# Optimization experiments

Hardware: AMD Instinct MI355X
Metric: run time of the kernel (lower is better)

Reference implementation:

```python
import jax, jax.numpy as jnp
import numpy as np

N_USERS = 100000
N_ITEMS = 50000
D = 128          # n_factors
L = 200          # hist_len
B = 2048
SIGMA = 0.1      # hyper_approx (posterior lognormal scale)
PRIOR = 1.0      # hyper_prior (prior lognormal scale)
TAU = 4.0
EPS = 1e-8
LN_EPS = 1e-5


def _layernorm(x, gamma, beta):
    m = jnp.mean(x, axis=-1, keepdims=True)
    v = jnp.var(x, axis=-1, keepdims=True)
    return (x - m) * jax.lax.rsqrt(v + LN_EPS) * gamma + beta


def setup_inputs() -> dict:
    key = jax.random.key(0)
    ks = jax.random.split(key, 20)
    user_idx = jax.random.randint(ks[0], (B,), 0, N_USERS, dtype=jnp.int32)
    item_idx = jax.random.randint(ks[1], (B,), 0, N_ITEMS, dtype=jnp.int32)
    # user_hist buffer: per-user ragged history padded with N_ITEMS
    lengths = jax.random.randint(ks[2], (N_USERS,), 1, L + 1, dtype=jnp.int32)
    raw_hist = jax.random.randint(ks[3], (N_USERS, L), 0, N_ITEMS, dtype=jnp.int32)
    pos = jnp.arange(L, dtype=jnp.int32)
    user_hist = jnp.where(pos[None, :] < lengths[:, None], raw_hist, N_ITEMS).astype(jnp.int32)
    # embeddings (padding rows zeroed, std=0.01 init)
    user_embed = 0.01 * jax.random.normal(ks[4], (N_USERS + 1, D), dtype=jnp.float32)
    user_embed = user_embed.at[N_USERS].set(0.0)
    item_embed = 0.01 * jax.random.normal(ks[5], (N_ITEMS + 1, D), dtype=jnp.float32)
    item_embed = item_embed.at[N_ITEMS].set(0.0)
    s = 1.0 / np.sqrt(D)
    W_i = s * jax.random.normal(ks[6], (D, D), dtype=jnp.float32)
    W_h = s * jax.random.normal(ks[7], (D, D), dtype=jnp.float32)
    # BAM 'concat' (additive) score params: v^T tanh(Wq q + Wk k)
    Wq = s * jax.random.normal(ks[8], (D, D), dtype=jnp.float32)
    Wk = s * jax.random.normal(ks[9], (D, D), dtype=jnp.float32)
    v_attn = s * jax.random.normal(ks[10], (D,), dtype=jnp.float32)
    pred_W = s * jax.random.normal(ks[11], (D,), dtype=jnp.float32)
    pred_b = jnp.zeros((), dtype=jnp.float32)
    gamma_u = jnp.ones((D,), jnp.float32); beta_u = jnp.zeros((D,), jnp.float32)
    gamma_i = jnp.ones((D,), jnp.float32); beta_i = jnp.zeros((D,), jnp.float32)
    # reparameterization noise (forward uses stochastic=True)
    noise_u = jax.random.normal(ks[12], (B, L), dtype=jnp.float32)
    noise_i = jax.random.normal(ks[13], (B, L), dtype=jnp.float32)
    return dict(user_idx=user_idx, item_idx=item_idx, user_hist=user_hist,
                user_embed=user_embed, item_embed=item_embed, W_i=W_i, W_h=W_h,
                Wq=Wq, Wk=Wk, v_attn=v_attn, pred_W=pred_W, pred_b=pred_b,
                gamma_u=gamma_u, beta_u=beta_u, gamma_i=gamma_i, beta_i=beta_i,
                noise_u=noise_u, noise_i=noise_i)


def reference(user_idx, item_idx, user_hist, user_embed, item_embed, W_i, W_h,
              Wq, Wk, v_attn, pred_W, pred_b, gamma_u, beta_u, gamma_i, beta_i,
              noise_u, noise_i):
    maskf_dummy = None  # (placeholder, no-op)
    hist = user_hist[user_idx]                                   # (B, L) int
    mask = (hist != item_idx[:, None]) & (hist != N_ITEMS)       # (B, L) bool
    maskf = mask.astype(jnp.float32)

    u_id = user_embed[user_idx]                                  # (B, D)
    t_raw = item_embed[item_idx]                                 # (B, D)
    h_raw = item_embed[hist]                                     # (B, L, D)
    t_id = t_raw @ W_i.T                                         # W_i(target)
    h_id = h_raw @ W_h.T                                         # W_h(hist)

    def bam(q, K, V, noise):
        # additive ('concat') scoring: v . tanh(q Wq + K Wk), temperature tau
        h = jnp.tanh((q @ Wq.T)[:, None, :] + jnp.einsum('bld,ed->ble', K, Wk))
        scores = jnp.einsum('ble,e->bl', h, v_attn) / TAU        # (B, L)
        scores = jnp.where(mask, scores, -1e9)
        phi = jax.nn.softmax(scores, axis=-1)                    # (B, L)
        mu = jnp.log(phi + EPS)
        w = jnp.exp(mu + SIGMA * noise) * maskf                  # lognormal sample
        attn = w / (jnp.sum(w, axis=-1, keepdims=True) + EPS)
        out = jnp.einsum('bl,bld->bd', attn, V)                  # (B, D)
        # KL( LN(mu, SIGMA) || LN(0, PRIOR) ) over valid positions
        kl_el = jnp.log(PRIOR / SIGMA) + (SIGMA ** 2 + mu ** 2) / (2.0 * PRIOR ** 2) - 0.5
        kl = jnp.sum(kl_el * maskf) / (jnp.sum(maskf) + EPS)
        return out, kl

    u_hist, kl_u = bam(u_id, h_id, h_id, noise_u)
    i_hist, kl_i = bam(t_id, h_id, h_id, noise_i)
    u = _layernorm(u_hist * u_id, gamma_u, beta_u)
    i = _layernorm(i_hist * t_id, gamma_i, beta_i)
    logit = (u * i) @ pred_W + pred_b                            # (B,)
    return logit, 0.5 * (kl_u + kl_i)
```

## Files before the change

kernel.cpp:

```cpp
#include <hip/hip_runtime.h>

#define B_ 2048
#define L_ 200
#define D_ 128
#define NITEMS 50000

typedef __attribute__((ext_vector_type(8))) short short8v;
typedef __attribute__((ext_vector_type(4))) float floatx4;
typedef __attribute__((ext_vector_type(4))) int intx4;

__device__ __forceinline__ short f2bf(float f) {
    union { float f; unsigned u; } v;
    v.f = f;
    unsigned r = v.u + 0x7FFFu + ((v.u >> 16) & 1u);
    return (short)(r >> 16);
}

__device__ __forceinline__ float tanh5(float x) {
    const float x2 = x * x;
    const float p = __builtin_fmaf(x2, 0.13333333f, -0.33333333f);
    return __builtin_fmaf(x * x2, p, x);
}

__device__ __forceinline__ float wave_sum(float v) {
#pragma unroll
    for (int m = 32; m >= 1; m >>= 1) v += __shfl_xor(v, m, 64);
    return v;
}

__device__ __forceinline__ void gload_lds16(const short* g, short* l) {
    __builtin_amdgcn_global_load_lds(
        (const __attribute__((address_space(1))) void*)g,
        (__attribute__((address_space(3))) void*)l, 16, 0, 0);
}

__device__ __forceinline__ intx4 ds_read16(const short* p) {
    intx4 d;
    asm volatile("ds_read_b128 %0, %1"
                 : "=v"(d)
                 : "v"((const __attribute__((address_space(3))) short*)p));
    return d;
}

__global__ __launch_bounds__(256) void k01(const float* __restrict__ Wk,
                                           const float* __restrict__ Wh,
                                           short* __restrict__ Mbf,
                                           const float* __restrict__ src,
                                           short* __restrict__ dst, int n8) {
    const int t = threadIdx.x;
    if (blockIdx.x < 128) {
        __shared__ float wk[128];
        const int e = blockIdx.x;
        if (t < 128) wk[t] = Wk[e * 128 + t];
        __syncthreads();
        if (t < 128) {
            float s = 0.f;
#pragma unroll 4
            for (int d = 0; d < 128; ++d) s += wk[d] * Wh[d * 128 + t];
            Mbf[e * 128 + t] = f2bf(s);
        }
        return;
    }
    const int i = (blockIdx.x - 128) * 256 + t;
    if (i >= n8) return;
    const float4 f0 = *reinterpret_cast<const float4*>(src + i * 8);
    const float4 f1 = *reinterpret_cast<const float4*>(src + i * 8 + 4);
    short8v w;
    w[0] = f2bf(f0.x); w[1] = f2bf(f0.y); w[2] = f2bf(f0.z); w[3] = f2bf(f0.w);
    w[4] = f2bf(f1.x); w[5] = f2bf(f1.y); w[6] = f2bf(f1.z); w[7] = f2bf(f1.w);
    *reinterpret_cast<short8v*>(dst + i * 8) = w;
}

__global__ __launch_bounds__(256) void k2_prep(
    const int* __restrict__ user_idx, const int* __restrict__ item_idx,
    const int* __restrict__ user_hist, const float* __restrict__ user_embed,
    const float* __restrict__ item_embed, const float* __restrict__ W_i,
    const float* __restrict__ Wq, float* __restrict__ uid_o,
    float* __restrict__ tid_o, float* __restrict__ qu_o, float* __restrict__ qt_o,
    int* __restrict__ hist_o) {
    const int bb = blockIdx.x * 4, t = threadIdx.x;
    __shared__ float uid_s[4][128], traw_s[4][128], tid_s[4][128];
    __shared__ int uis[4], iis[4];
    if (t < 4) {
        uis[t] = user_idx[bb + t];
        iis[t] = item_idx[bb + t];
    }
    __syncthreads();
#pragma unroll
    for (int c = 0; c < 2; ++c) {
        const int idx = c * 256 + t;
        const int bs = idx >> 7, e = idx & 127;
        const float uv = user_embed[(long)uis[bs] * 128 + e];
        uid_s[bs][e] = uv;
        traw_s[bs][e] = item_embed[(long)iis[bs] * 128 + e];
        uid_o[(bb + bs) * 128 + e] = uv;
    }
    for (int l0 = t; l0 < 800; l0 += 256) {
        const int bs = (l0 >= 200) + (l0 >= 400) + (l0 >= 600);
        hist_o[bb * 200 + l0] = user_hist[(long)uis[bs] * 200 + (l0 - bs * 200)];
    }
    __syncthreads();
    {
        const int half = t >> 7, e = t & 127;
        const float* Wrow = (half ? Wq : W_i) + e * 128;
        float acc[4] = {0.f, 0.f, 0.f, 0.f};
        for (int c = 0; c < 128; c += 4) {
            const float4 w = *reinterpret_cast<const float4*>(Wrow + c);
#pragma unroll
            for (int k = 0; k < 4; ++k) {
                const float4 s = half ? *reinterpret_cast<const float4*>(&uid_s[k][c])
                                      : *reinterpret_cast<const float4*>(&traw_s[k][c]);
                acc[k] += w.x * s.x + w.y * s.y + w.z * s.z + w.w * s.w;
            }
        }
#pragma unroll
        for (int k = 0; k < 4; ++k) {
            if (half) qu_o[(bb + k) * 128 + e] = acc[k];
            else {
                tid_s[k][e] = acc[k];
                tid_o[(bb + k) * 128 + e] = acc[k];
            }
        }
    }
    __syncthreads();
    {
        const int half = t >> 7, e = t & 127;
        const float* Wrow = Wq + e * 128;
        float acc[2] = {0.f, 0.f};
        for (int c = 0; c < 128; c += 4) {
            const float4 w = *reinterpret_cast<const float4*>(Wrow + c);
#pragma unroll
            for (int k = 0; k < 2; ++k) {
                const float4 s = *reinterpret_cast<const float4*>(&tid_s[half * 2 + k][c]);
                acc[k] += w.x * s.x + w.y * s.y + w.z * s.z + w.w * s.w;
            }
        }
#pragma unroll
        for (int k = 0; k < 2; ++k) qt_o[(bb + half * 2 + k) * 128 + e] = acc[k];
    }
}

__global__ __launch_bounds__(512) void k345(
    const short* __restrict__ Mbf, const short* __restrict__ item_bf,
    const int* __restrict__ hist_g, const int* __restrict__ item_idx,
    const float* __restrict__ qu_, const float* __restrict__ qt_,
    const float* __restrict__ v_attn, const float* __restrict__ noise_u,
    const float* __restrict__ noise_i, const float* __restrict__ W_h,
    const float* __restrict__ uid, const float* __restrict__ tid,
    const float* __restrict__ gamma_u, const float* __restrict__ beta_u,
    const float* __restrict__ gamma_i, const float* __restrict__ beta_i,
    const float* __restrict__ pred_W, const float* __restrict__ pred_b,
    float* __restrict__ klu, float* __restrict__ kli, float* __restrict__ msm,
    float* __restrict__ out) {
    __shared__ __align__(16) short M_lds[8][4][4][16][8];
    __shared__ __align__(16) char scratch[32768];
    __shared__ float q_lds[2][2][128];
    __shared__ float v_lds[128];
    __shared__ int hgs[400];
    __shared__ float scL[2 * 400];
    __shared__ float attL[2 * 400];
    __shared__ float red[8];

    const int t = threadIdx.x, blk = blockIdx.x;
    const int b0 = blk * 2;
    const int ii0 = item_idx[b0], ii1 = item_idx[b0 + 1];

#pragma unroll
    for (int c4 = 0; c4 < 4; ++c4) {
        const int flat = c4 * 512 + t;
        const int lo = flat & 15, g = (flat >> 4) & 3, ks = (flat >> 6) & 3, t8 = flat >> 8;
        *reinterpret_cast<short8v*>(&M_lds[t8][ks][g][lo][0]) =
            *reinterpret_cast<const short8v*>(Mbf + (t8 * 16 + lo) * 128 + ks * 32 + g * 8);
    }
    {
        const int bs = t >> 8, side = (t >> 7) & 1, e = t & 127;
        q_lds[bs][side][e] =
            side ? qt_[(b0 + bs) * 128 + e] : qu_[(b0 + bs) * 128 + e];
    }
    if (t < 128) v_lds[t] = v_attn[t];
    if (t < 400) hgs[t] = hist_g[blk * 400 + t];
    __syncthreads();

    const int wid = t >> 6, lane = t & 63;
    const int lo = lane & 15, hi = lane >> 4;

    {
        const int nt = (wid == 7) ? 4 : 3;
        short* wbase = reinterpret_cast<short*>(scratch) + wid * 2048;
        const char* itemc = (const char*)item_bf;

        int ro[4];
#pragma unroll
        for (int i = 0; i < 4; ++i) {
            const int lt = wid * 3 + ((i < 3) ? i : 3);
            ro[i] = hgs[min(lt, 24) * 16 + lo];
        }
        auto stage = [&](int i) {
            const char* rp = itemc + ((long)ro[i] << 8) + hi * 16;
#pragma unroll
            for (int ks = 0; ks < 4; ++ks)
                gload_lds16((const short*)(rp + ks * 64), wbase + ks * 512);
        };

        stage(0);
        for (int i = 0; i < nt; ++i) {
            asm volatile("s_waitcnt vmcnt(0)" ::: "memory");
            __builtin_amdgcn_sched_barrier(0);
            const short* pb = wbase + hi * 128 + lo * 8;
            intx4 r0 = ds_read16(pb);
            intx4 r1 = ds_read16(pb + 512);
            intx4 r2 = ds_read16(pb + 1024);
            intx4 r3 = ds_read16(pb + 1536);
            asm volatile("s_waitcnt lgkmcnt(0)" ::: "memory");
            __builtin_amdgcn_sched_barrier(0);
            short8v f[4];
            f[0] = __builtin_bit_cast(short8v, r0);
            f[1] = __builtin_bit_cast(short8v, r1);
            f[2] = __builtin_bit_cast(short8v, r2);
            f[3] = __builtin_bit_cast(short8v, r3);
            if (i + 1 < nt) stage(i + 1);
            __builtin_amdgcn_sched_barrier(0);

            const int lr = (wid * 3 + i) * 16 + lo;
            const int bs = lr >= 200;
            float su = 0.f, si = 0.f;
#pragma unroll
            for (int h2 = 0; h2 < 2; ++h2) {
                floatx4 acc[4];
#pragma unroll
                for (int q4 = 0; q4 < 4; ++q4) acc[q4] = (floatx4){0.f, 0.f, 0.f, 0.f};
#pragma unroll
                for (int ks = 0; ks < 4; ++ks)
#pragma unroll
                    for (int q4 = 0; q4 < 4; ++q4)
                        acc[q4] = __builtin_amdgcn_mfma_f32_16x16x32_bf16(
                            *reinterpret_cast<const short8v*>(&M_lds[h2 * 4 + q4][ks][hi][lo][0]),
                            f[ks], acc[q4], 0, 0, 0);
#pragma unroll
                for (int q4 = 0; q4 < 4; ++q4) {
                    const int t8 = h2 * 4 + q4;
                    const floatx4 vv = *reinterpret_cast<const floatx4*>(&v_lds[t8 * 16 + hi * 4]);
                    const floatx4 qa = *reinterpret_cast<const floatx4*>(&q_lds[bs][0][t8 * 16 + hi * 4]);
                    const floatx4 qb = *reinterpret_cast<const floatx4*>(&q_lds[bs][1][t8 * 16 + hi * 4]);
#pragma unroll
                    for (int rg = 0; rg < 4; ++rg) {
                        su = __builtin_fmaf(vv[rg], tanh5(qa[rg] + acc[q4][rg]), su);
                        si = __builtin_fmaf(vv[rg], tanh5(qb[rg] + acc[q4][rg]), si);
                    }
                }
            }
            su += __shfl_xor(su, 16, 64);
            su += __shfl_xor(su, 32, 64);
            si += __shfl_xor(si, 16, 64);
            si += __shfl_xor(si, 32, 64);
            if (hi == 0) {
                scL[lr] = su * 0.25f;
                scL[400 + lr] = si * 0.25f;
            }
        }
    }
    __syncthreads();

    if (wid < 4) {
        const int bs = wid & 1, side = wid >> 1;
        const int bb = b0 + bs;
        const int iiv = bs ? ii1 : ii0;
        const float* nz = (side ? noise_i : noise_u) + bb * L_;
        const float* scl = scL + side * 400 + bs * 200;
        const int* hrow = hgs + bs * 200;

        float mk[4], s2[4];
        float msl = 0.f, esum = 0.f;
#pragma unroll
        for (int k = 0; k < 4; ++k) {
            const int l = lane + 64 * k;
            const int hv = (l < L_) ? hrow[l] : NITEMS;
            mk[k] = (l < L_ && hv != iiv && hv != NITEMS) ? 1.f : 0.f;
            msl += mk[k];
            const float s = (mk[k] > 0.5f) ? scl[(l < L_) ? l : 0] : -1e9f;
            s2[k] = s * 1.4426950f;
            esum += exp2f(s2[k]);
        }
        const float msum = wave_sum(msl);
        float Z = wave_sum(esum);
        Z = fmaxf(Z, 1e-37f);
        const float z2 = log2f(Z);

        float wv[4], wsum = 0.f, klsum = 0.f;
#pragma unroll
        for (int k = 0; k < 4; ++k) {
            const int l = lane + 64 * k;
            const int lm = (l < L_) ? l : 0;
            const float d = s2[k] - z2;
            wv[k] = exp2f(__builtin_fmaf(nz[lm], 0.14426950f, d)) * mk[k];
            wsum += wv[k];
            klsum += (1.8075851f + 0.2402265f * d * d) * mk[k];
        }
        const float Zw = wave_sum(wsum);
        const float kls = wave_sum(klsum);
        const float invZw = 1.f / (Zw + 1e-8f);
#pragma unroll
        for (int k = 0; k < 4; ++k) {
            const int l = lane + 64 * k;
            if (l < L_) attL[side * 400 + bs * 200 + l] = wv[k] * invZw;
        }
        if (lane == 0) {
            if (side == 0) { klu[bb] = kls; msm[bb] = msum; }
            else kli[bb] = kls;
        }
    }
    __syncthreads();

    float* P = reinterpret_cast<float*>(scratch);
    {
        const int bs = wid >> 2, rg = wid & 3, c2 = lane;
        const float* a0p = attL + bs * 200;
        const float* a1p = attL + 400 + bs * 200;
        const int* hrow = hgs + bs * 200;
        float s00 = 0.f, s01 = 0.f, s10 = 0.f, s11 = 0.f;
#pragma unroll
        for (int c = 0; c < 2; ++c) {
            const int lb = rg * 50 + c * 25;
            unsigned hv[25];
#pragma unroll
            for (int j = 0; j < 25; ++j)
                hv[j] = *reinterpret_cast<const unsigned*>(
                    item_bf + (long)hrow[lb + j] * 128 + c2 * 2);
#pragma unroll
            for (int j = 0; j < 25; ++j) {
                const float h0 = __uint_as_float(hv[j] << 16);
                const float h1 = __uint_as_float(hv[j] & 0xffff0000u);
                const float a0 = a0p[lb + j], a1 = a1p[lb + j];
                s00 += a0 * h0; s01 += a0 * h1;
                s10 += a1 * h0; s11 += a1 * h1;
            }
        }
        P[((bs * 2 + 0) * 4 + rg) * 128 + c2 * 2] = s00;
        P[((bs * 2 + 0) * 4 + rg) * 128 + c2 * 2 + 1] = s01;
        P[((bs * 2 + 1) * 4 + rg) * 128 + c2 * 2] = s10;
        P[((bs * 2 + 1) * 4 + rg) * 128 + c2 * 2 + 1] = s11;
    }
    __syncthreads();

    const int bs3 = t >> 8, side3 = (t >> 7) & 1, tl = t & 127;
    const int grp = t >> 7;
    {
        const int gidx = (bs3 * 2 + side3) * 4;
        float a = P[(gidx + 0) * 128 + tl] + P[(gidx + 1) * 128 + tl] +
                  P[(gidx + 2) * 128 + tl] + P[(gidx + 3) * 128 + tl];
        __syncthreads();
        P[2048 + grp * 128 + tl] = a;
    }
    __syncthreads();

    float x;
    {
        const float* vsrc = P + 2048 + grp * 128;
        float o = 0.f;
#pragma unroll 2
        for (int c = 0; c < 128; c += 4) {
            const float4 w = *reinterpret_cast<const float4*>(&W_h[tl * 128 + c]);
            o += w.x * vsrc[c] + w.y * vsrc[c + 1] + w.z * vsrc[c + 2] + w.w * vsrc[c + 3];
        }
        x = o * (side3 ? tid[(b0 + bs3) * 128 + tl] : uid[(b0 + bs3) * 128 + tl]);
    }
    const float v1 = wave_sum(x);
    if (lane == 0) red[wid] = v1;
    __syncthreads();
    const float mean = (red[grp * 2] + red[grp * 2 + 1]) * (1.f / 128.f);
    const float d = x - mean;
    const float v2 = wave_sum(d * d);
    __syncthreads();
    if (lane == 0) red[wid] = v2;
    __syncthreads();
    const float var = (red[grp * 2] + red[grp * 2 + 1]) * (1.f / 128.f);
    const float gmm = side3 ? gamma_i[tl] : gamma_u[tl];
    const float bta = side3 ? beta_i[tl] : beta_u[tl];
    const float uin = d * rsqrtf(var + 1e-5f) * gmm + bta;
    __syncthreads();
    P[2560 + grp * 128 + tl] = uin;
    __syncthreads();
    float p = 0.f;
    if (t < 256) {
        const int bs = t >> 7, tl2 = t & 127;
        p = P[2560 + (bs * 2 + 0) * 128 + tl2] * P[2560 + (bs * 2 + 1) * 128 + tl2] *
            pred_W[tl2];
    }
    const float v3 = wave_sum(p);
    if (lane == 0 && wid < 4) red[4 + wid] = v3;
    __syncthreads();
    if (t == 0) out[b0] = red[4] + red[5] + pred_b[0];
    if (t == 1) out[b0 + 1] = red[6] + red[7] + pred_b[0];
}

__global__ __launch_bounds__(256) void k6_kl(const float* __restrict__ klu,
                                             const float* __restrict__ kli,
                                             const float* __restrict__ msm,
                                             float* __restrict__ out) {
    __shared__ float red[4];
    const int t = threadIdx.x;
    float su = 0.f, si = 0.f, sm = 0.f;
    for (int b = t; b < B_; b += 256) {
        su += klu[b];
        si += kli[b];
        sm += msm[b];
    }
    su = wave_sum(su);
    si = wave_sum(si);
    sm = wave_sum(sm);
    __syncthreads();
    if ((t & 63) == 0) red[t >> 6] = su;
    __syncthreads();
    su = red[0] + red[1] + red[2] + red[3];
    __syncthreads();
    if ((t & 63) == 0) red[t >> 6] = si;
    __syncthreads();
    si = red[0] + red[1] + red[2] + red[3];
    __syncthreads();
    if ((t & 63) == 0) red[t >> 6] = sm;
    __syncthreads();
    sm = red[0] + red[1] + red[2] + red[3];
    if (t == 0) {
        const float inv = 1.f / (sm + 1e-8f);
        out[0] = 0.5f * (su * inv + si * inv);
    }
}

extern "C" void kernel_launch(void* const* d_in, const int* in_sizes, int n_in,
                              void* d_out, int out_size, void* d_ws, size_t ws_size,
                              hipStream_t stream) {
    const int* user_idx = (const int*)d_in[0];
    const int* item_idx = (const int*)d_in[1];
    const int* user_hist = (const int*)d_in[2];
    const float* user_embed = (const float*)d_in[3];
    const float* item_embed = (const float*)d_in[4];
    const float* W_i = (const float*)d_in[5];
    const float* W_h = (const float*)d_in[6];
    const float* Wq = (const float*)d_in[7];
    const float* Wk = (const float*)d_in[8];
    const float* v_attn = (const float*)d_in[9];
    const float* pred_W = (const float*)d_in[10];
    const float* pred_b = (const float*)d_in[11];
    const float* gamma_u = (const float*)d_in[12];
    const float* beta_u = (const float*)d_in[13];
    const float* gamma_i = (const float*)d_in[14];
    const float* beta_i = (const float*)d_in[15];
    const float* noise_u = (const float*)d_in[16];
    const float* noise_i = (const float*)d_in[17];
    float* out = (float*)d_out;

    char* ws = (char*)d_ws;
    size_t off = 0;
    auto alloc = [&](size_t bytes) -> void* {
        void* p = ws + off;
        off = (off + bytes + 255) & ~(size_t)255;
        return p;
    };
    short* Mbf     = (short*)alloc(128 * 128 * 2);
    short* item_bf = (short*)alloc((size_t)(NITEMS + 1) * 128 * 2);
    float* uid = (float*)alloc((size_t)B_ * 128 * 4);
    float* tid = (float*)alloc((size_t)B_ * 128 * 4);
    float* qu  = (float*)alloc((size_t)B_ * 128 * 4);
    float* qt  = (float*)alloc((size_t)B_ * 128 * 4);
    int* hg    = (int*)alloc((size_t)B_ * L_ * 4);
    float* klu = (float*)alloc((size_t)B_ * 4);
    float* kli = (float*)alloc((size_t)B_ * 4);
    float* msm = (float*)alloc((size_t)B_ * 4);

    const int n8 = (NITEMS + 1) * 128 / 8;
    const int ncvt = (n8 + 255) / 256;
    k01<<<128 + ncvt, 256, 0, stream>>>(Wk, W_h, Mbf, item_embed, item_bf, n8);
    k2_prep<<<B_ / 4, 256, 0, stream>>>(user_idx, item_idx, user_hist, user_embed,
                                        item_embed, W_i, Wq, uid, tid, qu, qt, hg);
    k345<<<B_ / 2, 512, 0, stream>>>(Mbf, item_bf, hg, item_idx, qu, qt, v_attn,
                                     noise_u, noise_i, W_h, uid, tid, gamma_u, beta_u,
                                     gamma_i, beta_i, pred_W, pred_b, klu, kli, msm, out);
    k6_kl<<<1, 256, 0, stream>>>(klu, kli, msm, out + B_);
}
```

Baseline: 103.6 us.

## Merge prep kernels, prefetch history tiles early, single-pass layernorm stats

Merges the weight/item-conversion kernel and the per-batch prep kernel into one launch, removing a kernel boundary. In the main kernel, the first history-row tile is issued before the Mbf/q LDS setup, and half of the value-gather loads are hoisted ahead of the softmax phase so their latency overlaps other work. Layernorm now computes mean and E[x^2] in one reduction instead of two, dropping several barriers. The one-pass variance is less numerically robust, and the hoisted gather arrays add register pressure.

```diff
diff --git a/kernel.cpp b/kernel.cpp
--- a/kernel.cpp
+++ b/kernel.cpp
@@ -42,12 +42,18 @@
     return d;
 }
 
-__global__ __launch_bounds__(256) void k01(const float* __restrict__ Wk,
-                                           const float* __restrict__ Wh,
-                                           short* __restrict__ Mbf,
-                                           const float* __restrict__ src,
-                                           short* __restrict__ dst, int n8) {
+__global__ __launch_bounds__(256) void kprep(
+    const float* __restrict__ Wk, const float* __restrict__ Wh,
+    short* __restrict__ Mbf, const float* __restrict__ item_embed,
+    short* __restrict__ item_bf, int n8,
+    const int* __restrict__ user_idx, const int* __restrict__ item_idx,
+    const int* __restrict__ user_hist, const float* __restrict__ user_embed,
+    const float* __restrict__ W_i, const float* __restrict__ Wq,
+    float* __restrict__ uid_o, float* __restrict__ tid_o,
+    float* __restrict__ qu_o, float* __restrict__ qt_o, int* __restrict__ hist_o) {
     const int t = threadIdx.x;
+    const int ncvt = (n8 + 255) >> 8;
+
     if (blockIdx.x < 128) {
         __shared__ float wk[128];
         const int e = blockIdx.x;
@@ -61,24 +67,18 @@
         }
         return;
     }
-    const int i = (blockIdx.x - 128) * 256 + t;
-    if (i >= n8) return;
-    const float4 f0 = *reinterpret_cast<const float4*>(src + i * 8);
-    const float4 f1 = *reinterpret_cast<const float4*>(src + i * 8 + 4);
-    short8v w;
-    w[0] = f2bf(f0.x); w[1] = f2bf(f0.y); w[2] = f2bf(f0.z); w[3] = f2bf(f0.w);
-    w[4] = f2bf(f1.x); w[5] = f2bf(f1.y); w[6] = f2bf(f1.z); w[7] = f2bf(f1.w);
-    *reinterpret_cast<short8v*>(dst + i * 8) = w;
-}
-
-__global__ __launch_bounds__(256) void k2_prep(
-    const int* __restrict__ user_idx, const int* __restrict__ item_idx,
-    const int* __restrict__ user_hist, const float* __restrict__ user_embed,
-    const float* __restrict__ item_embed, const float* __restrict__ W_i,
-    const float* __restrict__ Wq, float* __restrict__ uid_o,
-    float* __restrict__ tid_o, float* __restrict__ qu_o, float* __restrict__ qt_o,
-    int* __restrict__ hist_o) {
-    const int bb = blockIdx.x * 4, t = threadIdx.x;
+    if (blockIdx.x < 128 + ncvt) {
+        const int i = (blockIdx.x - 128) * 256 + t;
+        if (i >= n8) return;
+        const float4 f0 = *reinterpret_cast<const float4*>(item_embed + i * 8);
+        const float4 f1 = *reinterpret_cast<const float4*>(item_embed + i * 8 + 4);
+        short8v w;
+        w[0] = f2bf(f0.x); w[1] = f2bf(f0.y); w[2] = f2bf(f0.z); w[3] = f2bf(f0.w);
+        w[4] = f2bf(f1.x); w[5] = f2bf(f1.y); w[6] = f2bf(f1.z); w[7] = f2bf(f1.w);
+        *reinterpret_cast<short8v*>(item_bf + i * 8) = w;
+        return;
+    }
+    const int bb = (blockIdx.x - 128 - ncvt) * 4;
     __shared__ float uid_s[4][128], traw_s[4][128], tid_s[4][128];
     __shared__ int uis[4], iis[4];
     if (t < 4) {
@@ -159,18 +159,36 @@
     __shared__ int hgs[400];
     __shared__ float scL[2 * 400];
     __shared__ float attL[2 * 400];
-    __shared__ float red[8];
+    __shared__ float red[8], red2[8];
 
     const int t = threadIdx.x, blk = blockIdx.x;
     const int b0 = blk * 2;
     const int ii0 = item_idx[b0], ii1 = item_idx[b0 + 1];
 
+    const int wid = t >> 6, lane = t & 63;
+    const int lo = lane & 15, hi = lane >> 4;
+
+    int ro[4];
+#pragma unroll
+    for (int i = 0; i < 4; ++i) {
+        const int lt = min(wid * 3 + ((i < 3) ? i : 3), 24);
+        ro[i] = hist_g[blk * 400 + lt * 16 + lo];
+    }
+    short* wbase = reinterpret_cast<short*>(scratch) + wid * 2048;
+    const char* itemc = (const char*)item_bf;
+    {
+        const char* rp = itemc + ((long)ro[0] << 8) + hi * 16;
+#pragma unroll
+        for (int ks = 0; ks < 4; ++ks)
+            gload_lds16((const short*)(rp + ks * 64), wbase + ks * 512);
+    }
+
 #pragma unroll
     for (int c4 = 0; c4 < 4; ++c4) {
         const int flat = c4 * 512 + t;
-        const int lo = flat & 15, g = (flat >> 4) & 3, ks = (flat >> 6) & 3, t8 = flat >> 8;
-        *reinterpret_cast<short8v*>(&M_lds[t8][ks][g][lo][0]) =
-            *reinterpret_cast<const short8v*>(Mbf + (t8 * 16 + lo) * 128 + ks * 32 + g * 8);
+        const int lo2 = flat & 15, g = (flat >> 4) & 3, ks = (flat >> 6) & 3, t8 = flat >> 8;
+        *reinterpret_cast<short8v*>(&M_lds[t8][ks][g][lo2][0]) =
+            *reinterpret_cast<const short8v*>(Mbf + (t8 * 16 + lo2) * 128 + ks * 32 + g * 8);
     }
     {
         const int bs = t >> 8, side = (t >> 7) & 1, e = t & 127;
@@ -181,20 +199,9 @@
     if (t < 400) hgs[t] = hist_g[blk * 400 + t];
     __syncthreads();
 
-    const int wid = t >> 6, lane = t & 63;
-    const int lo = lane & 15, hi = lane >> 4;
-
     {
         const int nt = (wid == 7) ? 4 : 3;
-        short* wbase = reinterpret_cast<short*>(scratch) + wid * 2048;
-        const char* itemc = (const char*)item_bf;
-
-        int ro[4];
-#pragma unroll
-        for (int i = 0; i < 4; ++i) {
-            const int lt = wid * 3 + ((i < 3) ? i : 3);
-            ro[i] = hgs[min(lt, 24) * 16 + lo];
-        }
+
         auto stage = [&](int i) {
             const char* rp = itemc + ((long)ro[i] << 8) + hi * 16;
 #pragma unroll
@@ -202,7 +209,6 @@
                 gload_lds16((const short*)(rp + ks * 64), wbase + ks * 512);
         };
 
-        stage(0);
         for (int i = 0; i < nt; ++i) {
             asm volatile("s_waitcnt vmcnt(0)" ::: "memory");
             __builtin_amdgcn_sched_barrier(0);
@@ -261,6 +267,15 @@
     }
     __syncthreads();
 
+    const int bsB = wid >> 2, rgB = wid & 3, c2 = lane;
+    const int* hrowB = hgs + bsB * 200;
+    unsigned hv0[25];
+#pragma unroll
+    for (int j = 0; j < 25; ++j)
+        hv0[j] = *reinterpret_cast<const unsigned*>(
+            item_bf + (long)hrowB[rgB * 50 + j] * 128 + c2 * 2);
+    __builtin_amdgcn_sched_barrier(0);
+
     if (wid < 4) {
         const int bs = wid & 1, side = wid >> 1;
         const int bb = b0 + bs;
@@ -313,32 +328,36 @@
 
     float* P = reinterpret_cast<float*>(scratch);
     {
-        const int bs = wid >> 2, rg = wid & 3, c2 = lane;
-        const float* a0p = attL + bs * 200;
-        const float* a1p = attL + 400 + bs * 200;
-        const int* hrow = hgs + bs * 200;
+        const float* a0p = attL + bsB * 200;
+        const float* a1p = attL + 400 + bsB * 200;
+        unsigned hv1[25];
+#pragma unroll
+        for (int j = 0; j < 25; ++j)
+            hv1[j] = *reinterpret_cast<const unsigned*>(
+                item_bf + (long)hrowB[rgB * 50 + 25 + j] * 128 + c2 * 2);
         float s00 = 0.f, s01 = 0.f, s10 = 0.f, s11 = 0.f;
 #pragma unroll
-        for (int c = 0; c < 2; ++c) {
-            const int lb = rg * 50 + c * 25;
-            unsigned hv[25];
-#pragma unroll
-            for (int j = 0; j < 25; ++j)
-                hv[j] = *reinterpret_cast<const unsigned*>(
-                    item_bf + (long)hrow[lb + j] * 128 + c2 * 2);
-#pragma unroll
-            for (int j = 0; j < 25; ++j) {
-                const float h0 = __uint_as_float(hv[j] << 16);
-                const float h1 = __uint_as_float(hv[j] & 0xffff0000u);
-                const float a0 = a0p[lb + j], a1 = a1p[lb + j];
-                s00 += a0 * h0; s01 += a0 * h1;
-                s10 += a1 * h0; s11 += a1 * h1;
-            }
-        }
-        P[((bs * 2 + 0) * 4 + rg) * 128 + c2 * 2] = s00;
-        P[((bs * 2 + 0) * 4 + rg) * 128 + c2 * 2 + 1] = s01;
-        P[((bs * 2 + 1) * 4 + rg) * 128 + c2 * 2] = s10;
-        P[((bs * 2 + 1) * 4 + rg) * 128 + c2 * 2 + 1] = s11;
+        for (int j = 0; j < 25; ++j) {
+            const float h0 = __uint_as_float(hv0[j] << 16);
+            const float h1 = __uint_as_float(hv0[j] & 0xffff0000u);
+            const int l = rgB * 50 + j;
+            const float a0 = a0p[l], a1 = a1p[l];
+            s00 += a0 * h0; s01 += a0 * h1;
+            s10 += a1 * h0; s11 += a1 * h1;
+        }
+#pragma unroll
+        for (int j = 0; j < 25; ++j) {
+            const float h0 = __uint_as_float(hv1[j] << 16);
+            const float h1 = __uint_as_float(hv1[j] & 0xffff0000u);
+            const int l = rgB * 50 + 25 + j;
+            const float a0 = a0p[l], a1 = a1p[l];
+            s00 += a0 * h0; s01 += a0 * h1;
+            s10 += a1 * h0; s11 += a1 * h1;
+        }
+        P[((bsB * 2 + 0) * 4 + rgB) * 128 + c2 * 2] = s00;
+        P[((bsB * 2 + 0) * 4 + rgB) * 128 + c2 * 2 + 1] = s01;
+        P[((bsB * 2 + 1) * 4 + rgB) * 128 + c2 * 2] = s10;
+        P[((bsB * 2 + 1) * 4 + rgB) * 128 + c2 * 2 + 1] = s11;
     }
     __syncthreads();
 
@@ -346,9 +365,8 @@
     const int grp = t >> 7;
     {
         const int gidx = (bs3 * 2 + side3) * 4;
-        float a = P[(gidx + 0) * 128 + tl] + P[(gidx + 1) * 128 + tl] +
-                  P[(gidx + 2) * 128 + tl] + P[(gidx + 3) * 128 + tl];
-        __syncthreads();
+        const float a = P[(gidx + 0) * 128 + tl] + P[(gidx + 1) * 128 + tl] +
+                        P[(gidx + 2) * 128 + tl] + P[(gidx + 3) * 128 + tl];
         P[2048 + grp * 128 + tl] = a;
     }
     __syncthreads();
@@ -357,7 +375,7 @@
     {
         const float* vsrc = P + 2048 + grp * 128;
         float o = 0.f;
-#pragma unroll 2
+#pragma unroll 8
         for (int c = 0; c < 128; c += 4) {
             const float4 w = *reinterpret_cast<const float4*>(&W_h[tl * 128 + c]);
             o += w.x * vsrc[c] + w.y * vsrc[c + 1] + w.z * vsrc[c + 2] + w.w * vsrc[c + 3];
@@ -365,19 +383,15 @@
         x = o * (side3 ? tid[(b0 + bs3) * 128 + tl] : uid[(b0 + bs3) * 128 + tl]);
     }
     const float v1 = wave_sum(x);
-    if (lane == 0) red[wid] = v1;
+    const float v2 = wave_sum(x * x);
+    if (lane == 0) { red[wid] = v1; red2[wid] = v2; }
     __syncthreads();
     const float mean = (red[grp * 2] + red[grp * 2 + 1]) * (1.f / 128.f);
-    const float d = x - mean;
-    const float v2 = wave_sum(d * d);
-    __syncthreads();
-    if (lane == 0) red[wid] = v2;
-    __syncthreads();
-    const float var = (red[grp * 2] + red[grp * 2 + 1]) * (1.f / 128.f);
+    const float ex2 = (red2[grp * 2] + red2[grp * 2 + 1]) * (1.f / 128.f);
+    const float var = __builtin_fmaf(-mean, mean, ex2);
     const float gmm = side3 ? gamma_i[tl] : gamma_u[tl];
     const float bta = side3 ? beta_i[tl] : beta_u[tl];
-    const float uin = d * rsqrtf(var + 1e-5f) * gmm + bta;
-    __syncthreads();
+    const float uin = (x - mean) * rsqrtf(var + 1e-5f) * gmm + bta;
     P[2560 + grp * 128 + tl] = uin;
     __syncthreads();
     float p = 0.f;
@@ -469,9 +483,9 @@
 
     const int n8 = (NITEMS + 1) * 128 / 8;
     const int ncvt = (n8 + 255) / 256;
-    k01<<<128 + ncvt, 256, 0, stream>>>(Wk, W_h, Mbf, item_embed, item_bf, n8);
-    k2_prep<<<B_ / 4, 256, 0, stream>>>(user_idx, item_idx, user_hist, user_embed,
-                                        item_embed, W_i, Wq, uid, tid, qu, qt, hg);
+    kprep<<<128 + ncvt + B_ / 4, 256, 0, stream>>>(
+        Wk, W_h, Mbf, item_embed, item_bf, n8, user_idx, item_idx, user_hist,
+        user_embed, W_i, Wq, uid, tid, qu, qt, hg);
     k345<<<B_ / 2, 512, 0, stream>>>(Mbf, item_bf, hg, item_idx, qu, qt, v_attn,
                                      noise_u, noise_i, W_h, uid, tid, gamma_u, beta_u,
                                      gamma_i, beta_i, pred_W, pred_b, klu, kli, msm, out);
```

Result: slower. 117.7 us (+13.7%).

## Shrink LDS footprint with half-row staging and bf16 score/attention buffers

Applied to the files above, without the earlier changes.

Staging of gathered item rows is split into two 128-byte halves per tile, halving the per-wave LDS staging buffer. A single 8-wide accumulator set is kept across all four k-slices. History indices become 16-bit, and scores and attention weights are stored as bf16 in one shared buffer that is reused in place. Together these cut LDS use per block, probably to fit more blocks per CU. The cost is extra vmcnt waits inside each tile, which reduce load/compute overlap, and precision loss from rounding scores and attention weights to bf16.

```diff
diff --git a/kernel.cpp b/kernel.cpp
--- a/kernel.cpp
+++ b/kernel.cpp
@@ -14,6 +14,11 @@
     v.f = f;
     unsigned r = v.u + 0x7FFFu + ((v.u >> 16) & 1u);
     return (short)(r >> 16);
+}
+__device__ __forceinline__ float bf2f(unsigned short s) {
+    union { unsigned u; float f; } v;
+    v.u = ((unsigned)s) << 16;
+    return v.f;
 }
 
 __device__ __forceinline__ float tanh5(float x) {
@@ -153,12 +158,11 @@
     float* __restrict__ klu, float* __restrict__ kli, float* __restrict__ msm,
     float* __restrict__ out) {
     __shared__ __align__(16) short M_lds[8][4][4][16][8];
-    __shared__ __align__(16) char scratch[32768];
+    __shared__ __align__(16) char scratch[16384];
     __shared__ float q_lds[2][2][128];
     __shared__ float v_lds[128];
-    __shared__ int hgs[400];
-    __shared__ float scL[2 * 400];
-    __shared__ float attL[2 * 400];
+    __shared__ unsigned short hgs[400];
+    __shared__ unsigned short scA[800];
     __shared__ float red[8];
 
     const int t = threadIdx.x, blk = blockIdx.x;
@@ -168,9 +172,9 @@
 #pragma unroll
     for (int c4 = 0; c4 < 4; ++c4) {
         const int flat = c4 * 512 + t;
-        const int lo = flat & 15, g = (flat >> 4) & 3, ks = (flat >> 6) & 3, t8 = flat >> 8;
-        *reinterpret_cast<short8v*>(&M_lds[t8][ks][g][lo][0]) =
-            *reinterpret_cast<const short8v*>(Mbf + (t8 * 16 + lo) * 128 + ks * 32 + g * 8);
+        const int lo2 = flat & 15, g = (flat >> 4) & 3, ks = (flat >> 6) & 3, t8 = flat >> 8;
+        *reinterpret_cast<short8v*>(&M_lds[t8][ks][g][lo2][0]) =
+            *reinterpret_cast<const short8v*>(Mbf + (t8 * 16 + lo2) * 128 + ks * 32 + g * 8);
     }
     {
         const int bs = t >> 8, side = (t >> 7) & 1, e = t & 127;
@@ -178,7 +182,7 @@
             side ? qt_[(b0 + bs) * 128 + e] : qu_[(b0 + bs) * 128 + e];
     }
     if (t < 128) v_lds[t] = v_attn[t];
-    if (t < 400) hgs[t] = hist_g[blk * 400 + t];
+    if (t < 400) hgs[t] = (unsigned short)hist_g[blk * 400 + t];
     __syncthreads();
 
     const int wid = t >> 6, lane = t & 63;
@@ -186,67 +190,82 @@
 
     {
         const int nt = (wid == 7) ? 4 : 3;
-        short* wbase = reinterpret_cast<short*>(scratch) + wid * 2048;
+        short* wbase = reinterpret_cast<short*>(scratch) + wid * 1024;
         const char* itemc = (const char*)item_bf;
 
         int ro[4];
 #pragma unroll
         for (int i = 0; i < 4; ++i) {
-            const int lt = wid * 3 + ((i < 3) ? i : 3);
-            ro[i] = hgs[min(lt, 24) * 16 + lo];
-        }
-        auto stage = [&](int i) {
-            const char* rp = itemc + ((long)ro[i] << 8) + hi * 16;
-#pragma unroll
-            for (int ks = 0; ks < 4; ++ks)
-                gload_lds16((const short*)(rp + ks * 64), wbase + ks * 512);
+            const int lt = min(wid * 3 + ((i < 3) ? i : 3), 24);
+            ro[i] = (int)hgs[lt * 16 + lo];
+        }
+        auto stage_half = [&](int i, int h) {
+            const char* rp = itemc + ((long)ro[i] << 8) + hi * 16 + h * 128;
+            gload_lds16((const short*)rp, wbase);
+            gload_lds16((const short*)(rp + 64), wbase + 512);
         };
 
-        stage(0);
+        stage_half(0, 0);
         for (int i = 0; i < nt; ++i) {
+            floatx4 acc[8];
+#pragma unroll
+            for (int t8 = 0; t8 < 8; ++t8) acc[t8] = (floatx4){0.f, 0.f, 0.f, 0.f};
+            const short* pb = wbase + hi * 128 + lo * 8;
+
             asm volatile("s_waitcnt vmcnt(0)" ::: "memory");
             __builtin_amdgcn_sched_barrier(0);
-            const short* pb = wbase + hi * 128 + lo * 8;
             intx4 r0 = ds_read16(pb);
             intx4 r1 = ds_read16(pb + 512);
-            intx4 r2 = ds_read16(pb + 1024);
-            intx4 r3 = ds_read16(pb + 1536);
             asm volatile("s_waitcnt lgkmcnt(0)" ::: "memory");
             __builtin_amdgcn_sched_barrier(0);
-            short8v f[4];
-            f[0] = __builtin_bit_cast(short8v, r0);
-            f[1] = __builtin_bit_cast(short8v, r1);
-            f[2] = __builtin_bit_cast(short8v, r2);
-            f[3] = __builtin_bit_cast(short8v, r3);
-            if (i + 1 < nt) stage(i + 1);
-            __builtin_amdgcn_sched_barrier(0);
+            short8v f0 = __builtin_bit_cast(short8v, r0);
+            short8v f1 = __builtin_bit_cast(short8v, r1);
+            stage_half(i, 1);
+            __builtin_amdgcn_sched_barrier(0);
+#pragma unroll
+            for (int t8 = 0; t8 < 8; ++t8)
+                acc[t8] = __builtin_amdgcn_mfma_f32_16x16x32_bf16(
+                    *reinterpret_cast<const short8v*>(&M_lds[t8][0][hi][lo][0]), f0,
+                    acc[t8], 0, 0, 0);
+#pragma unroll
+            for (int t8 = 0; t8 < 8; ++t8)
+                acc[t8] = __builtin_amdgcn_mfma_f32_16x16x32_bf16(
+                    *reinterpret_cast<const short8v*>(&M_lds[t8][1][hi][lo][0]), f1,
+                    acc[t8], 0, 0, 0);
+
+            asm volatile("s_waitcnt vmcnt(0)" ::: "memory");
+            __builtin_amdgcn_sched_barrier(0);
+            intx4 r2 = ds_read16(pb);
+            intx4 r3 = ds_read16(pb + 512);
+            asm volatile("s_waitcnt lgkmcnt(0)" ::: "memory");
+            __builtin_amdgcn_sched_barrier(0);
+            short8v f2 = __builtin_bit_cast(short8v, r2);
+            short8v f3 = __builtin_bit_cast(short8v, r3);
+            if (i + 1 < nt) stage_half(i + 1, 0);
+            __builtin_amdgcn_sched_barrier(0);
+#pragma unroll
+            for (int t8 = 0; t8 < 8; ++t8)
+                acc[t8] = __builtin_amdgcn_mfma_f32_16x16x32_bf16(
+                    *reinterpret_cast<const short8v*>(&M_lds[t8][2][hi][lo][0]), f2,
+                    acc[t8], 0, 0, 0);
+#pragma unroll
+            for (int t8 = 0; t8 < 8; ++t8)
+                acc[t8] = __builtin_amdgcn_mfma_f32_16x16x32_bf16(
+                    *reinterpret_cast<const short8v*>(&M_lds[t8][3][hi][lo][0]), f3,
+                    acc[t8], 0, 0, 0);
 
             const int lr = (wid * 3 + i) * 16 + lo;
             const int bs = lr >= 200;
             float su = 0.f, si = 0.f;
 #pragma unroll
-            for (int h2 = 0; h2 < 2; ++h2) {
-                floatx4 acc[4];
-#pragma unroll
-                for (int q4 = 0; q4 < 4; ++q4) acc[q4] = (floatx4){0.f, 0.f, 0.f, 0.f};
-#pragma unroll
-                for (int ks = 0; ks < 4; ++ks)
-#pragma unroll
-                    for (int q4 = 0; q4 < 4; ++q4)
-                        acc[q4] = __builtin_amdgcn_mfma_f32_16x16x32_bf16(
-                            *reinterpret_cast<const short8v*>(&M_lds[h2 * 4 + q4][ks][hi][lo][0]),
-                            f[ks], acc[q4], 0, 0, 0);
-#pragma unroll
-                for (int q4 = 0; q4 < 4; ++q4) {
-                    const int t8 = h2 * 4 + q4;
-                    const floatx4 vv = *reinterpret_cast<const floatx4*>(&v_lds[t8 * 16 + hi * 4]);
-                    const floatx4 qa = *reinterpret_cast<const floatx4*>(&q_lds[bs][0][t8 * 16 + hi * 4]);
-                    const floatx4 qb = *reinterpret_cast<const floatx4*>(&q_lds[bs][1][t8 * 16 + hi * 4]);
-#pragma unroll
-                    for (int rg = 0; rg < 4; ++rg) {
-                        su = __builtin_fmaf(vv[rg], tanh5(qa[rg] + acc[q4][rg]), su);
-                        si = __builtin_fmaf(vv[rg], tanh5(qb[rg] + acc[q4][rg]), si);
-                    }
+            for (int t8 = 0; t8 < 8; ++t8) {
+                const floatx4 vv = *reinterpret_cast<const floatx4*>(&v_lds[t8 * 16 + hi * 4]);
+                const floatx4 qa = *reinterpret_cast<const floatx4*>(&q_lds[bs][0][t8 * 16 + hi * 4]);
+                const floatx4 qb = *reinterpret_cast<const floatx4*>(&q_lds[bs][1][t8 * 16 + hi * 4]);
+#pragma unroll
+                for (int rg = 0; rg < 4; ++rg) {
+                    su = __builtin_fmaf(vv[rg], tanh5(qa[rg] + acc[t8][rg]), su);
+                    si = __builtin_fmaf(vv[rg], tanh5(qb[rg] + acc[t8][rg]), si);
                 }
             }
             su += __shfl_xor(su, 16, 64);
@@ -254,8 +273,8 @@
             si += __shfl_xor(si, 16, 64);
             si += __shfl_xor(si, 32, 64);
             if (hi == 0) {
-                scL[lr] = su * 0.25f;
-                scL[400 + lr] = si * 0.25f;
+                scA[lr] = (unsigned short)f2bf(su * 0.25f);
+                scA[400 + lr] = (unsigned short)f2bf(si * 0.25f);
             }
         }
     }
@@ -266,18 +285,18 @@
         const int bb = b0 + bs;
         const int iiv = bs ? ii1 : ii0;
         const float* nz = (side ? noise_i : noise_u) + bb * L_;
-        const float* scl = scL + side * 400 + bs * 200;
-        const int* hrow = hgs + bs * 200;
+        unsigned short* scl = scA + side * 400 + bs * 200;
+        const unsigned short* hrow = hgs + bs * 200;
 
         float mk[4], s2[4];
         float msl = 0.f, esum = 0.f;
 #pragma unroll
         for (int k = 0; k < 4; ++k) {
             const int l = lane + 64 * k;
-            const int hv = (l < L_) ? hrow[l] : NITEMS;
+            const int hv = (l < L_) ? (int)hrow[l] : NITEMS;
             mk[k] = (l < L_ && hv != iiv && hv != NITEMS) ? 1.f : 0.f;
             msl += mk[k];
-            const float s = (mk[k] > 0.5f) ? scl[(l < L_) ? l : 0] : -1e9f;
+            const float s = (mk[k] > 0.5f) ? bf2f(scl[(l < L_) ? l : 0]) : -1e9f;
             s2[k] = s * 1.4426950f;
             esum += exp2f(s2[k]);
         }
@@ -302,7 +321,7 @@
 #pragma unroll
         for (int k = 0; k < 4; ++k) {
             const int l = lane + 64 * k;
-            if (l < L_) attL[side * 400 + bs * 200 + l] = wv[k] * invZw;
+            if (l < L_) scl[l] = (unsigned short)f2bf(wv[k] * invZw);
         }
         if (lane == 0) {
             if (side == 0) { klu[bb] = kls; msm[bb] = msum; }
@@ -314,9 +333,9 @@
     float* P = reinterpret_cast<float*>(scratch);
     {
         const int bs = wid >> 2, rg = wid & 3, c2 = lane;
-        const float* a0p = attL + bs * 200;
-        const float* a1p = attL + 400 + bs * 200;
-        const int* hrow = hgs + bs * 200;
+        const unsigned short* a0p = scA + bs * 200;
+        const unsigned short* a1p = scA + 400 + bs * 200;
+        const unsigned short* hrow = hgs + bs * 200;
         float s00 = 0.f, s01 = 0.f, s10 = 0.f, s11 = 0.f;
 #pragma unroll
         for (int c = 0; c < 2; ++c) {
@@ -330,7 +349,8 @@
             for (int j = 0; j < 25; ++j) {
                 const float h0 = __uint_as_float(hv[j] << 16);
                 const float h1 = __uint_as_float(hv[j] & 0xffff0000u);
-                const float a0 = a0p[lb + j], a1 = a1p[lb + j];
+                const float a0 = bf2f(a0p[lb + j]);
+                const float a1 = bf2f(a1p[lb + j]);
                 s00 += a0 * h0; s01 += a0 * h1;
                 s10 += a1 * h0; s11 += a1 * h1;
             }
```

After: 105.7 us. 1.02x slower.
